# Optimization experiments

Measured on AMD Instinct MI355X. Metric: run time of the kernel, lower is better.

The kernel has to match this reference:

```python
import jax, jax.numpy as jnp
import numpy as np

N = 50000      # nodes
E = 800000     # edges (before self loops)
NFEAT = 128
HEADS = 4
NCLASS = 32    # per-head out channels of each GATConv
NHID = HEADS * NCLASS  # 128, inter-layer width
NEG_SLOPE = 0.2


def setup_inputs() -> dict:
    key = jax.random.key(0)
    ks = jax.random.split(key, 10)
    x = jax.random.normal(ks[0], (N, NFEAT), dtype=jnp.float32)
    adj = jax.random.randint(ks[1], (2, E), 0, N, dtype=jnp.int32)

    def glorot(k, shape):
        fan = shape[0] + shape[-1]
        return jax.random.normal(k, shape, dtype=jnp.float32) * jnp.sqrt(2.0 / fan)

    # conv1: nfeat -> heads*nclass
    W1 = glorot(ks[2], (NFEAT, HEADS * NCLASS))
    att_src1 = glorot(ks[3], (HEADS, NCLASS))
    att_dst1 = glorot(ks[4], (HEADS, NCLASS))
    b1 = jnp.zeros((HEADS * NCLASS,), dtype=jnp.float32)
    # conv2: nhid -> heads*nclass
    W2 = glorot(ks[5], (NHID, HEADS * NCLASS))
    att_src2 = glorot(ks[6], (HEADS, NCLASS))
    att_dst2 = glorot(ks[7], (HEADS, NCLASS))
    b2 = jnp.zeros((HEADS * NCLASS,), dtype=jnp.float32)
    return {"x": x, "adj": adj,
            "W1": W1, "att_src1": att_src1, "att_dst1": att_dst1, "b1": b1,
            "W2": W2, "att_src2": att_src2, "att_dst2": att_dst2, "b2": b2}


def gat_conv(x, src, dst, n, W, att_src, att_dst, bias):
    """PyG GATConv (concat=True, inference): gather -> edge attention -> segment softmax -> scatter."""
    H, C = att_src.shape
    h = (x @ W).reshape(n, H, C)                    # [N,H,C]
    a_s = jnp.sum(h * att_src[None], axis=-1)       # [N,H]
    a_d = jnp.sum(h * att_dst[None], axis=-1)       # [N,H]
    e = jax.nn.leaky_relu(a_s[src] + a_d[dst], NEG_SLOPE)  # [E,H]
    # numerically-stable segment softmax over edges grouped by destination node
    m = jax.ops.segment_max(e, dst, num_segments=n)        # [N,H]
    m = jnp.where(jnp.isfinite(m), m, 0.0)
    ex = jnp.exp(e - m[dst])                               # [E,H]
    denom = jax.ops.segment_sum(ex, dst, num_segments=n)   # [N,H]
    alpha = ex / (denom[dst] + 1e-16)                      # [E,H]
    out = jax.ops.segment_sum(h[src] * alpha[:, :, None], dst, num_segments=n)  # [N,H,C]
    return out.reshape(n, H * C) + bias


def reference(x, adj, W1, att_src1, att_dst1, b1, W2, att_src2, att_dst2, b2):
    # PyG GATConv adds self loops by default
    loops = jnp.arange(N, dtype=adj.dtype)
    src = jnp.concatenate([adj[0], loops])
    dst = jnp.concatenate([adj[1], loops])
    h = jax.nn.relu(gat_conv(x, src, dst, N, W1, att_src1, att_dst1, b1))
    # dropout is identity in eval mode
    out = gat_conv(h, src, dst, N, W2, att_src2, att_dst2, b2)
    return out
```

## Files before the change

kernel.cpp:

```cpp
#include <hip/hip_runtime.h>
#include <hip/hip_fp16.h>

#define N_NODES 50000
#define E_EDGES 800000
#define ETOT    (E_EDGES + N_NODES)
#define NF      128
#define HEADS   4
#define NC      32
#define LOG2E   1.44269504088896340736f
#define ASTRIDE 136
#define CAP     96

#define NBUCK   196
#define EPB     4096
#define NBLKA   ((ETOT + EPB - 1) / EPB)
#define PARTN   (NBUCK * NBLKA)
#define NBLKS   ((PARTN + 255) / 256)
#define WCB     65

typedef __attribute__((ext_vector_type(8))) short short8v;
typedef __attribute__((ext_vector_type(4))) float f32x4;

__device__ inline ushort rne_bf16(float x) {
    uint u = __float_as_uint(x);
    return (ushort)((u + 0x7fff + ((u >> 16) & 1)) >> 16);
}
__device__ inline float h2f_lo(uint u) { return __half2float(__ushort_as_half((ushort)(u & 0xffffu))); }
__device__ inline float h2f_hi(uint u) { return __half2float(__ushort_as_half((ushort)(u >> 16))); }

__device__ inline void wconv_body(int wb, int tid, const float* __restrict__ W,
                                  const float* __restrict__ att_src,
                                  const float* __restrict__ att_dst,
                                  ushort* __restrict__ Wt) {
    if (wb < 64) {
        int i = wb * 256 + tid;
        int k = i >> 7, n = i & 127;
        Wt[n * 144 + k] = rne_bf16(W[i]);
    } else {
        for (int j = tid; j < 1024; j += 256) {
            int k = j >> 3, o = j & 7;
            int h = o & 3;
            const float* av = (o < 4) ? att_src : att_dst;
            float s = 0.f;
            #pragma unroll
            for (int c = 0; c < 32; ++c) s += W[k * 128 + h * 32 + c] * av[h * 32 + c];
            Wt[(128 + o) * 144 + k] = rne_bf16(s * LOG2E);
        }
        for (int j = tid; j < 8 * 144; j += 256)
            Wt[(136 + (j / 144)) * 144 + (j % 144)] = 0;
    }
}

__global__ __launch_bounds__(256) void prep_kernel(const int* __restrict__ adj,
                                                   int* __restrict__ partials,
                                                   const float* __restrict__ W1,
                                                   const float* __restrict__ as1,
                                                   const float* __restrict__ ad1,
                                                   ushort* __restrict__ Wt1,
                                                   const float* __restrict__ W2,
                                                   const float* __restrict__ as2,
                                                   const float* __restrict__ ad2,
                                                   ushort* __restrict__ Wt2) {
    __shared__ int lc[NBUCK];
    int b = blockIdx.x, tid = threadIdx.x;
    if (b < NBLKA) {
        for (int i = tid; i < NBUCK; i += 256) lc[i] = 0;
        __syncthreads();
        int base = b * EPB;
        #pragma unroll
        for (int i = 0; i < EPB / 256; ++i) {
            int e = base + i * 256 + tid;
            if (e < ETOT) {
                int dst = (e < E_EDGES) ? adj[E_EDGES + e] : (e - E_EDGES);
                atomicAdd(&lc[dst >> 8], 1);
            }
        }
        __syncthreads();
        for (int i = tid; i < NBUCK; i += 256) partials[i * NBLKA + b] = lc[i];
    } else {
        int wb = b - NBLKA;
        if (wb < WCB) wconv_body(wb, tid, W1, as1, ad1, Wt1);
        else          wconv_body(wb - WCB, tid, W2, as2, ad2, Wt2);
    }
}

__device__ inline int block_incl_scan(int v, int* sh4) {
    int lane = threadIdx.x & 63, wid = threadIdx.x >> 6;
    int s = v;
    #pragma unroll
    for (int ofs = 1; ofs < 64; ofs <<= 1) {
        int t = __shfl_up(s, ofs);
        if (lane >= ofs) s += t;
    }
    if (lane == 63) sh4[wid] = s;
    __syncthreads();
    int add = 0;
    #pragma unroll
    for (int k = 0; k < 3; ++k) if (k < wid) add += sh4[k];
    return s + add;
}

__global__ __launch_bounds__(256) void bsum2_kernel(const int* __restrict__ partials,
                                                    int* __restrict__ bsum) {
    __shared__ int sh4[4];
    int i = blockIdx.x * 256 + threadIdx.x;
    int v = (i < PARTN) ? partials[i] : 0;
    int s = block_incl_scan(v, sh4);
    if (threadIdx.x == 255) bsum[blockIdx.x] = s;
}

__global__ __launch_bounds__(256) void scan_bsums2_kernel(const int* __restrict__ bsum,
                                                          int* __restrict__ bofs) {
    __shared__ int sh4[4];
    int i = threadIdx.x;
    int v = (i < NBLKS) ? bsum[i] : 0;
    int s = block_incl_scan(v, sh4);
    if (i < NBLKS) bofs[i] = s - v;
}

__global__ __launch_bounds__(256) void scan_final2_kernel(const int* __restrict__ partials,
                                                          const int* __restrict__ bofs,
                                                          int* __restrict__ pscan) {
    __shared__ int sh4[4];
    int i = blockIdx.x * 256 + threadIdx.x;
    int v = (i < PARTN) ? partials[i] : 0;
    int s = block_incl_scan(v, sh4);
    if (i < PARTN) pscan[i] = bofs[blockIdx.x] + s - v;
}

__global__ __launch_bounds__(256) void pass_scatter_kernel(const int* __restrict__ adj,
                                                           const int* __restrict__ pscan,
                                                           int2* __restrict__ ebuf) {
    __shared__ int lc[NBUCK];
    int tid = threadIdx.x;
    for (int i = tid; i < NBUCK; i += 256) lc[i] = 0;
    __syncthreads();
    int base = blockIdx.x * EPB;
    #pragma unroll
    for (int i = 0; i < EPB / 256; ++i) {
        int e = base + i * 256 + tid;
        if (e < ETOT) {
            int src, dst;
            if (e < E_EDGES) { src = adj[e]; dst = adj[E_EDGES + e]; }
            else             { src = dst = e - E_EDGES; }
            int b = dst >> 8;
            int r = atomicAdd(&lc[b], 1);
            ebuf[pscan[b * NBLKA + blockIdx.x] + r] = make_int2(src, dst);
        }
    }
}

__global__ __launch_bounds__(256) void pass_build_kernel(const int2* __restrict__ ebuf,
                                                         const int* __restrict__ pscan,
                                                         int* __restrict__ cnt,
                                                         int* __restrict__ slots) {
    __shared__ int lc[256];
    int tid = threadIdx.x;
    int b = blockIdx.x;
    lc[tid] = 0;
    __syncthreads();
    int base = pscan[b * NBLKA];
    int end  = (b == NBUCK - 1) ? ETOT : pscan[(b + 1) * NBLKA];
    for (int e = base + tid; e < end; e += 256) {
        int2 sd = ebuf[e];
        int d = sd.y & 255;
        int r = atomicAdd(&lc[d], 1);
        slots[(size_t)sd.y * CAP + r] = sd.x;
    }
    __syncthreads();
    int dst = b * 256 + tid;
    if (dst < N_NODES) cnt[dst] = lc[tid];
}

__global__ __launch_bounds__(256) void gemm_mfma_kernel(const float* __restrict__ X,
                                                        const ushort* __restrict__ Wt,
                                                        ushort* __restrict__ Hf,
                                                        float* __restrict__ a_s,
                                                        float* __restrict__ a_d, int nrows) {
    __shared__ ushort Abf[64 * ASTRIDE];
    int tid = threadIdx.x;
    int r0 = blockIdx.x * 64;

    {
        const float4* Xv = (const float4*)(X + (size_t)r0 * NF);
        int rleft = nrows - r0;
        #pragma unroll
        for (int p = 0; p < 8; ++p) {
            int i = p * 256 + tid;
            int row = i >> 5, c4 = i & 31;
            float4 v = (row < rleft) ? Xv[row * 32 + c4] : make_float4(0.f, 0.f, 0.f, 0.f);
            ushort4 hv;
            hv.x = rne_bf16(v.x); hv.y = rne_bf16(v.y);
            hv.z = rne_bf16(v.z); hv.w = rne_bf16(v.w);
            *(ushort4*)&Abf[row * ASTRIDE + c4 * 4] = hv;
        }
    }
    __syncthreads();

    int wv = tid >> 6;
    int l = tid & 63;
    int lr = l & 15;
    int lk = l >> 4;
    int rowb = wv * 16;

    short8v a[4];
    #pragma unroll
    for (int kc = 0; kc < 4; ++kc)
        a[kc] = *(const short8v*)&Abf[(rowb + lr) * ASTRIDE + kc * 32 + lk * 8];

    f32x4 acc[9];
    #pragma unroll
    for (int ct = 0; ct < 9; ++ct) acc[ct] = (f32x4){0.f, 0.f, 0.f, 0.f};

    #pragma unroll
    for (int ct = 0; ct < 9; ++ct) {
        #pragma unroll
        for (int kc = 0; kc < 4; ++kc) {
            short8v b = *(const short8v*)&Wt[(ct * 16 + lr) * 144 + kc * 32 + lk * 8];
            acc[ct] = __builtin_amdgcn_mfma_f32_16x16x32_bf16(a[kc], b, acc[ct], 0, 0, 0);
        }
    }

    int rbase = r0 + rowb + lk * 4;
    #pragma unroll
    for (int ct = 0; ct < 8; ++ct) {
        int col = ct * 16 + lr;
        #pragma unroll
        for (int ri = 0; ri < 4; ++ri) {
            int r = rbase + ri;
            if (r < nrows) Hf[(size_t)r * NF + col] = __half_as_ushort(__float2half(acc[ct][ri]));
        }
    }
    if (lr < 8) {
        #pragma unroll
        for (int ri = 0; ri < 4; ++ri) {
            int r = rbase + ri;
            if (r < nrows) {
                if (lr < 4) a_s[(size_t)r * 4 + lr] = acc[8][ri];
                else        a_d[(size_t)r * 4 + (lr - 4)] = acc[8][ri];
            }
        }
    }
}

__global__ __launch_bounds__(256) void agg_kernel(const ushort* __restrict__ Hf,
                                                  const float* __restrict__ a_s,
                                                  const float* __restrict__ a_d,
                                                  const int* __restrict__ cnt,
                                                  const int* __restrict__ slots,
                                                  const float* __restrict__ bias,
                                                  float* __restrict__ Out, int relu) {
    int lane = threadIdx.x & 63;
    int node = blockIdx.x * 4 + (threadIdx.x >> 6);
    if (node >= N_NODES) return;
    int q = lane >> 4;
    int t = lane & 15;
    int h = t >> 2;
    float adn = a_d[node * 4 + h];
    int deg = cnt[node];
    const int* row = slots + (size_t)node * CAP;
    const uint4* H4 = (const uint4*)Hf;
    float acc[8];
    #pragma unroll
    for (int k = 0; k < 8; ++k) acc[k] = 0.f;
    float denom = 0.f;

    for (int j = 0; j < deg; j += 8) {
        int sv[2]; float ev[2]; uint4 hv[2]; bool ok[2];
        #pragma unroll
        for (int u = 0; u < 2; ++u) {
            int idx = j + u * 4 + q;
            ok[u] = idx < deg;
            sv[u] = row[ok[u] ? idx : 0];
        }
        #pragma unroll
        for (int u = 0; u < 2; ++u) ev[u] = a_s[sv[u] * 4 + h];
        #pragma unroll
        for (int u = 0; u < 2; ++u) hv[u] = H4[(size_t)sv[u] * 16 + t];
        #pragma unroll
        for (int u = 0; u < 2; ++u) {
            float e = ev[u] + adn;
            e = (e > 0.f) ? e : 0.2f * e;
            float w = ok[u] ? exp2f(e) : 0.f;
            denom += w;
            acc[0] = fmaf(h2f_lo(hv[u].x), w, acc[0]);
            acc[1] = fmaf(h2f_hi(hv[u].x), w, acc[1]);
            acc[2] = fmaf(h2f_lo(hv[u].y), w, acc[2]);
            acc[3] = fmaf(h2f_hi(hv[u].y), w, acc[3]);
            acc[4] = fmaf(h2f_lo(hv[u].z), w, acc[4]);
            acc[5] = fmaf(h2f_hi(hv[u].z), w, acc[5]);
            acc[6] = fmaf(h2f_lo(hv[u].w), w, acc[6]);
            acc[7] = fmaf(h2f_hi(hv[u].w), w, acc[7]);
        }
    }
    #pragma unroll
    for (int ofs = 16; ofs < 64; ofs <<= 1) {
        denom += __shfl_xor(denom, ofs);
        #pragma unroll
        for (int k = 0; k < 8; ++k) acc[k] += __shfl_xor(acc[k], ofs);
    }
    if (q == 0) {
        float inv = 1.f / (denom + 1e-16f);
        float4 b0 = ((const float4*)bias)[t * 2];
        float4 b1 = ((const float4*)bias)[t * 2 + 1];
        float4 o0 = make_float4(acc[0] * inv + b0.x, acc[1] * inv + b0.y,
                                acc[2] * inv + b0.z, acc[3] * inv + b0.w);
        float4 o1 = make_float4(acc[4] * inv + b1.x, acc[5] * inv + b1.y,
                                acc[6] * inv + b1.z, acc[7] * inv + b1.w);
        if (relu) {
            o0.x = fmaxf(o0.x, 0.f); o0.y = fmaxf(o0.y, 0.f);
            o0.z = fmaxf(o0.z, 0.f); o0.w = fmaxf(o0.w, 0.f);
            o1.x = fmaxf(o1.x, 0.f); o1.y = fmaxf(o1.y, 0.f);
            o1.z = fmaxf(o1.z, 0.f); o1.w = fmaxf(o1.w, 0.f);
        }
        float4* orow = (float4*)(Out + (size_t)node * NF);
        orow[t * 2]     = o0;
        orow[t * 2 + 1] = o1;
    }
}

extern "C" void kernel_launch(void* const* d_in, const int* in_sizes, int n_in,
                              void* d_out, int out_size, void* d_ws, size_t ws_size,
                              hipStream_t stream) {
    const float* x        = (const float*)d_in[0];
    const int*   adj      = (const int*)  d_in[1];
    const float* W1       = (const float*)d_in[2];
    const float* att_src1 = (const float*)d_in[3];
    const float* att_dst1 = (const float*)d_in[4];
    const float* b1       = (const float*)d_in[5];
    const float* W2       = (const float*)d_in[6];
    const float* att_src2 = (const float*)d_in[7];
    const float* att_dst2 = (const float*)d_in[8];
    const float* b2       = (const float*)d_in[9];
    float* out = (float*)d_out;

    float* obuf = (float*)d_ws;
    float* a_s  = obuf + (size_t)N_NODES * NF;
    float* a_d  = a_s + (size_t)N_NODES * HEADS;
    ushort* Hf  = (ushort*)(a_d + (size_t)N_NODES * HEADS);
    ushort* Wt1 = Hf + (size_t)N_NODES * NF;
    ushort* Wt2 = Wt1 + 144 * 144;
    int* cnt     = (int*)(Wt2 + 144 * 144);
    int* slots   = cnt + N_NODES;
    int* partials= slots + (size_t)N_NODES * CAP;
    int* pscan   = partials + PARTN;
    int* bsum    = pscan + PARTN;
    int* bofs    = bsum + NBLKS;
    int2* ebuf   = (int2*)(bofs + NBLKS + 2);

    prep_kernel<<<NBLKA + 2 * WCB, 256, 0, stream>>>(adj, partials,
                                                     W1, att_src1, att_dst1, Wt1,
                                                     W2, att_src2, att_dst2, Wt2);
    bsum2_kernel<<<NBLKS, 256, 0, stream>>>(partials, bsum);
    scan_bsums2_kernel<<<1, 256, 0, stream>>>(bsum, bofs);
    scan_final2_kernel<<<NBLKS, 256, 0, stream>>>(partials, bofs, pscan);
    pass_scatter_kernel<<<NBLKA, 256, 0, stream>>>(adj, pscan, ebuf);
    pass_build_kernel<<<NBUCK, 256, 0, stream>>>(ebuf, pscan, cnt, slots);

    gemm_mfma_kernel<<<(N_NODES + 63) / 64, 256, 0, stream>>>(x, Wt1, Hf, a_s, a_d, N_NODES);
    agg_kernel<<<(N_NODES + 3) / 4, 256, 0, stream>>>(Hf, a_s, a_d, cnt, slots, b1, obuf, 1);

    gemm_mfma_kernel<<<(N_NODES + 63) / 64, 256, 0, stream>>>(obuf, Wt2, Hf, a_s, a_d, N_NODES);
    agg_kernel<<<(N_NODES + 3) / 4, 256, 0, stream>>>(Hf, a_s, a_d, cnt, slots, b2, out, 0);
}
```

Baseline: 149.7 us.

## Store projected features head-major and split aggregation across heads

The GEMM now writes the fp16 projected features in a head-major layout ([head][node][32]) instead of row-major [node][128]. The aggregation kernel launches four times as many blocks, each handling one head per node, with 8 edges in flight per wave and 8-byte gathers. The aim is to raise parallelism and shrink each gathered slice so a head's feature table is more cache-resident. In exchange, each edge's slot index and a_s value are now loaded once per head instead of once overall, and gathers are narrower.

New measurement: 249.1 us. 1.66x slower.

```diff
diff --git a/kernel.cpp b/kernel.cpp
--- a/kernel.cpp
+++ b/kernel.cpp
@@ -225,10 +225,12 @@
     #pragma unroll
     for (int ct = 0; ct < 8; ++ct) {
         int col = ct * 16 + lr;
+        int hd = col >> 5, cc = col & 31;
+        ushort* Hslice = Hf + (size_t)hd * N_NODES * 32 + cc;
         #pragma unroll
         for (int ri = 0; ri < 4; ++ri) {
             int r = rbase + ri;
-            if (r < nrows) Hf[(size_t)r * NF + col] = __half_as_ushort(__float2half(acc[ct][ri]));
+            if (r < nrows) Hslice[(size_t)r * 32] = __half_as_ushort(__float2half(acc[ct][ri]));
         }
     }
     if (lr < 8) {
@@ -250,72 +252,51 @@
                                                   const int* __restrict__ slots,
                                                   const float* __restrict__ bias,
                                                   float* __restrict__ Out, int relu) {
+    int bid = blockIdx.x;
+    int hb = bid & 3;
+    int node = (bid >> 2) * 4 + (threadIdx.x >> 6);
+    if (node >= N_NODES) return;
     int lane = threadIdx.x & 63;
-    int node = blockIdx.x * 4 + (threadIdx.x >> 6);
-    if (node >= N_NODES) return;
-    int q = lane >> 4;
-    int t = lane & 15;
-    int h = t >> 2;
-    float adn = a_d[node * 4 + h];
+    int es = lane >> 3;
+    int f = lane & 7;
+    float adn = a_d[node * 4 + hb];
     int deg = cnt[node];
     const int* row = slots + (size_t)node * CAP;
-    const uint4* H4 = (const uint4*)Hf;
-    float acc[8];
-    #pragma unroll
-    for (int k = 0; k < 8; ++k) acc[k] = 0.f;
+    const uint2* H2 = (const uint2*)(Hf + (size_t)hb * N_NODES * 32);
+    float acc[4] = {0.f, 0.f, 0.f, 0.f};
     float denom = 0.f;
 
     for (int j = 0; j < deg; j += 8) {
-        int sv[2]; float ev[2]; uint4 hv[2]; bool ok[2];
-        #pragma unroll
-        for (int u = 0; u < 2; ++u) {
-            int idx = j + u * 4 + q;
-            ok[u] = idx < deg;
-            sv[u] = row[ok[u] ? idx : 0];
-        }
-        #pragma unroll
-        for (int u = 0; u < 2; ++u) ev[u] = a_s[sv[u] * 4 + h];
-        #pragma unroll
-        for (int u = 0; u < 2; ++u) hv[u] = H4[(size_t)sv[u] * 16 + t];
-        #pragma unroll
-        for (int u = 0; u < 2; ++u) {
-            float e = ev[u] + adn;
-            e = (e > 0.f) ? e : 0.2f * e;
-            float w = ok[u] ? exp2f(e) : 0.f;
-            denom += w;
-            acc[0] = fmaf(h2f_lo(hv[u].x), w, acc[0]);
-            acc[1] = fmaf(h2f_hi(hv[u].x), w, acc[1]);
-            acc[2] = fmaf(h2f_lo(hv[u].y), w, acc[2]);
-            acc[3] = fmaf(h2f_hi(hv[u].y), w, acc[3]);
-            acc[4] = fmaf(h2f_lo(hv[u].z), w, acc[4]);
-            acc[5] = fmaf(h2f_hi(hv[u].z), w, acc[5]);
-            acc[6] = fmaf(h2f_lo(hv[u].w), w, acc[6]);
-            acc[7] = fmaf(h2f_hi(hv[u].w), w, acc[7]);
-        }
-    }
-    #pragma unroll
-    for (int ofs = 16; ofs < 64; ofs <<= 1) {
+        int idx = j + es;
+        bool ok = idx < deg;
+        int sv = row[ok ? idx : 0];
+        float ev = a_s[sv * 4 + hb];
+        uint2 hv = H2[(size_t)sv * 8 + f];
+        float e = ev + adn;
+        e = (e > 0.f) ? e : 0.2f * e;
+        float w = ok ? exp2f(e) : 0.f;
+        denom += w;
+        acc[0] = fmaf(h2f_lo(hv.x), w, acc[0]);
+        acc[1] = fmaf(h2f_hi(hv.x), w, acc[1]);
+        acc[2] = fmaf(h2f_lo(hv.y), w, acc[2]);
+        acc[3] = fmaf(h2f_hi(hv.y), w, acc[3]);
+    }
+    #pragma unroll
+    for (int ofs = 8; ofs < 64; ofs <<= 1) {
         denom += __shfl_xor(denom, ofs);
         #pragma unroll
-        for (int k = 0; k < 8; ++k) acc[k] += __shfl_xor(acc[k], ofs);
-    }
-    if (q == 0) {
+        for (int k = 0; k < 4; ++k) acc[k] += __shfl_xor(acc[k], ofs);
+    }
+    if (es == 0) {
         float inv = 1.f / (denom + 1e-16f);
-        float4 b0 = ((const float4*)bias)[t * 2];
-        float4 b1 = ((const float4*)bias)[t * 2 + 1];
-        float4 o0 = make_float4(acc[0] * inv + b0.x, acc[1] * inv + b0.y,
-                                acc[2] * inv + b0.z, acc[3] * inv + b0.w);
-        float4 o1 = make_float4(acc[4] * inv + b1.x, acc[5] * inv + b1.y,
-                                acc[6] * inv + b1.z, acc[7] * inv + b1.w);
+        float4 bv = ((const float4*)bias)[hb * 8 + f];
+        float4 o = make_float4(acc[0] * inv + bv.x, acc[1] * inv + bv.y,
+                               acc[2] * inv + bv.z, acc[3] * inv + bv.w);
         if (relu) {
-            o0.x = fmaxf(o0.x, 0.f); o0.y = fmaxf(o0.y, 0.f);
-            o0.z = fmaxf(o0.z, 0.f); o0.w = fmaxf(o0.w, 0.f);
-            o1.x = fmaxf(o1.x, 0.f); o1.y = fmaxf(o1.y, 0.f);
-            o1.z = fmaxf(o1.z, 0.f); o1.w = fmaxf(o1.w, 0.f);
-        }
-        float4* orow = (float4*)(Out + (size_t)node * NF);
-        orow[t * 2]     = o0;
-        orow[t * 2 + 1] = o1;
+            o.x = fmaxf(o.x, 0.f); o.y = fmaxf(o.y, 0.f);
+            o.z = fmaxf(o.z, 0.f); o.w = fmaxf(o.w, 0.f);
+        }
+        ((float4*)(Out + (size_t)node * NF))[hb * 8 + f] = o;
     }
 }
 
@@ -357,9 +338,10 @@
     pass_scatter_kernel<<<NBLKA, 256, 0, stream>>>(adj, pscan, ebuf);
     pass_build_kernel<<<NBUCK, 256, 0, stream>>>(ebuf, pscan, cnt, slots);
 
+    int aggblocks = 4 * ((N_NODES + 3) / 4);
     gemm_mfma_kernel<<<(N_NODES + 63) / 64, 256, 0, stream>>>(x, Wt1, Hf, a_s, a_d, N_NODES);
-    agg_kernel<<<(N_NODES + 3) / 4, 256, 0, stream>>>(Hf, a_s, a_d, cnt, slots, b1, obuf, 1);
+    agg_kernel<<<aggblocks, 256, 0, stream>>>(Hf, a_s, a_d, cnt, slots, b1, obuf, 1);
 
     gemm_mfma_kernel<<<(N_NODES + 63) / 64, 256, 0, stream>>>(obuf, Wt2, Hf, a_s, a_d, N_NODES);
-    agg_kernel<<<(N_NODES + 3) / 4, 256, 0, stream>>>(Hf, a_s, a_d, cnt, slots, b2, out, 0);
-}
+    agg_kernel<<<aggblocks, 256, 0, stream>>>(Hf, a_s, a_d, cnt, slots, b2, out, 0);
+}
```
